# Optimization experiments

Measured on AMD Instinct MI355X. Metric: run time of the kernel, lower is better.

Reference implementation:

```python
import jax, jax.numpy as jnp
import numpy as np

N = 50000      # nodes
E = 600000     # edges
F_IN = 128
F_OUT = 128
R = 4          # num_relations
BN_EPS = 1e-5  # PyTorch BatchNorm1d default


def setup_inputs() -> dict:
    key = jax.random.key(0)
    ks = jax.random.split(key, 8)
    s = 1.0 / np.sqrt(F_IN)
    return {
        "x": jax.random.normal(ks[0], (N, F_IN), jnp.float32),
        "edge_index": jax.random.randint(ks[1], (2, E), 0, N),
        "edge_type": jax.random.randint(ks[2], (E,), 0, R),
        "W_self": jax.random.uniform(ks[3], (F_IN, F_OUT), jnp.float32, -s, s),
        "b_self": jnp.zeros((F_OUT,), jnp.float32),
        "W1": jax.random.uniform(ks[4], (R, F_IN, F_OUT), jnp.float32, -s, s),
        "b1": jnp.zeros((R, F_OUT), jnp.float32),
        "gamma": jnp.ones((R, F_OUT), jnp.float32),
        "beta": jnp.zeros((R, F_OUT), jnp.float32),
        "W2": jax.random.uniform(ks[5], (R, F_OUT, F_OUT), jnp.float32, -s, s),
        "b2": jnp.zeros((R, F_OUT), jnp.float32),
    }


def reference(x, edge_index, edge_type, W_self, b_self, W1, b1, gamma, beta, W2, b2):
    row, col = edge_index[0], edge_index[1]
    # Per-relation scatter-add aggregation in one segment_sum pass:
    # segment id = relation * N + destination row.
    seg = edge_type * N + row
    agg = jax.ops.segment_sum(x[col], seg, num_segments=R * N)
    agg = agg.reshape(R, N, F_IN)
    # GIN update with eps=0: h_r = x + agg_r
    h = x[None, :, :] + agg                              # (R, N, F_IN)
    # Per-relation MLP: Linear -> BatchNorm(train stats) -> ReLU -> Linear
    h = jnp.einsum('rnf,rfo->rno', h, W1) + b1[:, None, :]
    mean = jnp.mean(h, axis=1, keepdims=True)
    var = jnp.var(h, axis=1, keepdims=True)              # biased, as in BN
    h = (h - mean) * jax.lax.rsqrt(var + BN_EPS)
    h = h * gamma[:, None, :] + beta[:, None, :]
    h = jax.nn.relu(h)
    h = jnp.einsum('rno,rop->rnp', h, W2) + b2[:, None, :]
    # Self-loop linear plus sum over relations
    return x @ W_self + b_self + jnp.sum(h, axis=0)
```

## Files before the change

### kernel.cpp

```cpp
#include <hip/hip_runtime.h>

#define Nn 50000
#define Ee 600000
#define Rr 4
#define BN_EPS 1e-5f
#define RCAP 10
#define OVFCAP 256
#define MCAP 128

typedef __bf16 bfrag  __attribute__((ext_vector_type(8)));
typedef float  f32x4  __attribute__((ext_vector_type(4)));

__device__ __forceinline__ unsigned short f2b(float f) {
    union { float f; unsigned int u; } v; v.f = f;
    return (unsigned short)((v.u + 0x7FFFu + ((v.u >> 16) & 1u)) >> 16);
}
__device__ __forceinline__ float b2f(unsigned short u) {
    union { unsigned int u; float f; } v; v.u = ((unsigned int)u) << 16; return v.f;
}

__global__ __launch_bounds__(256) void prep_k(
    const float* __restrict__ x, const float* __restrict__ W1,
    const float* __restrict__ W2, const float* __restrict__ Wself,
    const int* __restrict__ ei, const int* __restrict__ et,
    unsigned int* __restrict__ xb, unsigned short* __restrict__ WT,
    int* __restrict__ rowcnt, unsigned short* __restrict__ bkt,
    int* __restrict__ ovf)
{
    int b = blockIdx.x;
    if (b < 12500) {
        int i = b * 256 + threadIdx.x;
        float2 v = ((const float2*)x)[i];
        xb[i] = ((unsigned int)f2b(v.y) << 16) | f2b(v.x);
    } else if (b < 13076) {
        int idx = (b - 12500) * 256 + threadIdx.x;
        int mat = idx >> 14, rem = idx & 16383;
        int n = rem >> 7, k = rem & 127;
        const float* src = (mat < 4) ? (W1 + mat * 16384)
                         : (mat < 8) ? (W2 + (mat - 4) * 16384) : Wself;
        WT[idx] = f2b(src[k * 128 + n]);
    } else {
        int e = (b - 13076) * 256 + threadIdx.x;
        if (e < Ee) {
            int dst = ei[e], rel = et[e], src = ei[Ee + e];
            int bin = rel * Nn + dst;
            int pos = atomicAdd(&rowcnt[bin], 1);
            if (pos < RCAP) {
                bkt[(size_t)bin * RCAP + pos] = (unsigned short)src;
            } else {
                int op = atomicAdd(&ovf[0], 1);
                if (op < OVFCAP) { ovf[2 + op * 2] = bin; ovf[3 + op * 2] = src; }
            }
        }
    }
}

#define ACC_QUAD(u0_, u1_, u2_, u3_)                                      \
    do {                                                                  \
        unsigned int uu[16] = {u0_.x,u0_.y,u0_.z,u0_.w, u1_.x,u1_.y,u1_.z,u1_.w, \
                               u2_.x,u2_.y,u2_.z,u2_.w, u3_.x,u3_.y,u3_.z,u3_.w}; \
        _Pragma("unroll")                                                 \
        for (int jj = 0; jj < 16; ++jj) {                                 \
            acc[2*jj]   += b2f((unsigned short)(uu[jj] & 0xFFFF));        \
            acc[2*jj+1] += b2f((unsigned short)(uu[jj] >> 16));           \
        }                                                                 \
    } while (0)

__global__ __launch_bounds__(512) void gemm1f_k(
    const unsigned int* __restrict__ xb, const int* __restrict__ rowcnt,
    const unsigned short* __restrict__ bkt, const int* __restrict__ ovf,
    const unsigned short* __restrict__ WT,
    const float* __restrict__ b1, unsigned short* __restrict__ h,
    float* __restrict__ gsum, float* __restrict__ gsq)
{
    const int r  = blockIdx.y;
    const int n0 = blockIdx.x * 128;
    const int t  = threadIdx.x;

    __shared__ __attribute__((aligned(16))) __bf16 As[128][136];
    __shared__ __attribute__((aligned(16))) __bf16 Ws[128][136];
    __shared__ float s_sum[128], s_sq[128];
    __shared__ int s_cnt[128];
    __shared__ int s_edge[128 * RCAP];
    __shared__ int s_mrow[MCAP], s_msrc[MCAP];
    __shared__ int s_on, s_nm;

    const int rows = (Nn - n0 < 128) ? (Nn - n0) : 128;
    const int base = r * Nn + n0;
    if (t < 128) {
        s_sum[t] = 0.f; s_sq[t] = 0.f;
        int c = (t < rows) ? rowcnt[base + t] : 0;
        s_cnt[t] = (c < RCAP) ? c : RCAP;
    }
    {
        const unsigned short* Wr = WT + r * 16384;
        for (int i = t; i < 2048; i += 512) {
            int n = i >> 4, kc = (i & 15) << 3;
            *(uint4*)&Ws[n][kc] = *(const uint4*)(Wr + n * 128 + kc);
        }
    }
    {
        const unsigned int* bp = (const unsigned int*)(bkt + (size_t)base * RCAP);
        for (int i = t; i < (128 * RCAP) / 2; i += 512) {
            int row = i / (RCAP / 2);
            unsigned int u = (row < rows) ? bp[i] : 0u;
            s_edge[2 * i]     = (int)(u & 0xFFFFu);
            s_edge[2 * i + 1] = (int)(u >> 16);
        }
    }
    if (t == 0) {
        int on = ovf[0];
        s_on = (on < OVFCAP) ? on : OVFCAP;
        s_nm = 0;
    }
    __syncthreads();
    if (t < s_on) {
        int bin = ovf[2 + t * 2];
        if (bin >= base && bin < base + rows) {
            int k = atomicAdd(&s_nm, 1);
            if (k < MCAP) { s_mrow[k] = bin - base; s_msrc[k] = ovf[3 + t * 2]; }
        }
    }
    __syncthreads();
    const int nm = (s_nm < MCAP) ? s_nm : MCAP;

    {
        const int row = t >> 2, q = t & 3, gm = n0 + row;
        float acc[32];
#pragma unroll
        for (int j = 0; j < 32; ++j) acc[j] = 0.f;
        if (gm < Nn) {
            const uint4* xr = (const uint4*)(xb + (size_t)gm * 64 + q * 16);
            uint4 u0 = xr[0], u1 = xr[1], u2 = xr[2], u3 = xr[3];
            ACC_QUAD(u0, u1, u2, u3);
            const int je = s_cnt[row];
            const int rb = row * RCAP;
            if (je > 0) {
#define EIDX(jj) (s_edge[rb + ((jj) < je ? (jj) : (je - 1))])
#define EPTR(jj) ((const uint4*)(xb + (size_t)EIDX(jj) * 64 + q * 16))
                const uint4* pA = EPTR(0);
                const uint4* pB = EPTR(1);
                const uint4* pC = EPTR(2);
                uint4 A0 = pA[0], A1 = pA[1], A2 = pA[2], A3 = pA[3];
                uint4 B0 = pB[0], B1 = pB[1], B2 = pB[2], B3 = pB[3];
                uint4 C0 = pC[0], C1 = pC[1], C2 = pC[2], C3 = pC[3];
                for (int j = 0; j < je; j += 3) {
                    ACC_QUAD(A0, A1, A2, A3);
                    { const uint4* p = EPTR(j + 3); A0 = p[0]; A1 = p[1]; A2 = p[2]; A3 = p[3]; }
                    if (j + 1 < je) ACC_QUAD(B0, B1, B2, B3);
                    { const uint4* p = EPTR(j + 4); B0 = p[0]; B1 = p[1]; B2 = p[2]; B3 = p[3]; }
                    if (j + 2 < je) ACC_QUAD(C0, C1, C2, C3);
                    { const uint4* p = EPTR(j + 5); C0 = p[0]; C1 = p[1]; C2 = p[2]; C3 = p[3]; }
                }
#undef EIDX
#undef EPTR
            }
            for (int i = 0; i < nm; ++i) {
                if (s_mrow[i] == row) {
                    const uint4* p = (const uint4*)(xb + (size_t)s_msrc[i] * 64 + q * 16);
                    uint4 o0 = p[0], o1 = p[1], o2 = p[2], o3 = p[3];
                    ACC_QUAD(o0, o1, o2, o3);
                }
            }
        }
        unsigned int pk[16];
#pragma unroll
        for (int j = 0; j < 16; ++j)
            pk[j] = ((unsigned int)f2b(acc[2*j+1]) << 16) | f2b(acc[2*j]);
        uint4* dst = (uint4*)&As[row][q * 32];
        dst[0] = make_uint4(pk[0],  pk[1],  pk[2],  pk[3]);
        dst[1] = make_uint4(pk[4],  pk[5],  pk[6],  pk[7]);
        dst[2] = make_uint4(pk[8],  pk[9],  pk[10], pk[11]);
        dst[3] = make_uint4(pk[12], pk[13], pk[14], pk[15]);
    }
    __syncthreads();

    const int w = t >> 6, l = t & 63, ln = l & 15, quad = l >> 4;
    f32x4 acc2[8];
#pragma unroll
    for (int c = 0; c < 8; ++c) acc2[c] = (f32x4){0.f,0.f,0.f,0.f};
#pragma unroll
    for (int kk = 0; kk < 4; ++kk) {
        int ks = kk * 32 + quad * 8;
        bfrag a = *(const bfrag*)&As[w * 16 + ln][ks];
#pragma unroll
        for (int c = 0; c < 8; ++c) {
            bfrag b = *(const bfrag*)&Ws[c * 16 + ln][ks];
            acc2[c] = __builtin_amdgcn_mfma_f32_16x16x32_bf16(a, b, acc2[c], 0, 0, 0);
        }
    }
    __syncthreads();

#pragma unroll
    for (int c = 0; c < 8; ++c) {
        int col = c * 16 + ln;
        float bias = b1[r * 128 + col];
        float ps = 0.f, pq = 0.f;
#pragma unroll
        for (int reg = 0; reg < 4; ++reg) {
            int lrow = w * 16 + quad * 4 + reg;
            float v = acc2[c][reg] + bias;
            As[lrow][col] = (__bf16)v;
            if (n0 + lrow < Nn) { ps += v; pq += v * v; }
        }
        ps += __shfl_xor(ps, 16); pq += __shfl_xor(pq, 16);
        ps += __shfl_xor(ps, 32); pq += __shfl_xor(pq, 32);
        if (quad == 0) { atomicAdd(&s_sum[col], ps); atomicAdd(&s_sq[col], pq); }
    }
    __syncthreads();

    unsigned short* hr = h + (size_t)r * Nn * 128;
    for (int i = t; i < 2048; i += 512) {
        int m = i >> 4, kc = (i & 15) << 3;
        int gm = n0 + m;
        if (gm < Nn) *(uint4*)(hr + (size_t)gm * 128 + kc) = *(const uint4*)&As[m][kc];
    }
    if (t < 128) {
        atomicAdd(&gsum[r * 128 + t], s_sum[t]);
        atomicAdd(&gsq[r * 128 + t],  s_sq[t]);
    }
}

__global__ void finalize_k(
    const float* __restrict__ gsum, const float* __restrict__ gsq,
    const float* __restrict__ gamma, const float* __restrict__ beta,
    float* __restrict__ coefA, float* __restrict__ coefC)
{
    int i = threadIdx.x;
    float mean = gsum[i] * (1.0f / Nn);
    float var  = gsq[i] * (1.0f / Nn) - mean * mean;
    float a    = gamma[i] * rsqrtf(fmaxf(var, 0.f) + BN_EPS);
    coefA[i] = a;
    coefC[i] = beta[i] - mean * a;
}

__global__ __launch_bounds__(512) void gemm2f_k(
    const unsigned int* __restrict__ xb,
    const unsigned short* __restrict__ h,
    const unsigned short* __restrict__ WT,
    const float* __restrict__ bself, const float* __restrict__ b2,
    const float* __restrict__ coefA, const float* __restrict__ coefC,
    float* __restrict__ out)
{
    const int n0 = blockIdx.x * 128;
    const int t  = threadIdx.x;
    __shared__ __attribute__((aligned(16))) __bf16 As[128][136];
    __shared__ __attribute__((aligned(16))) __bf16 Ws[128][136];

    const int w = t >> 6, l = t & 63, ln = l & 15, quad = l >> 4;
    f32x4 acc2[8];
#pragma unroll
    for (int c = 0; c < 8; ++c) acc2[c] = (f32x4){0.f,0.f,0.f,0.f};

    for (int rr = 0; rr < 5; ++rr) {
        const unsigned short* Wr = WT + (rr < 4 ? (4 + rr) : 8) * 16384;
        for (int i = t; i < 2048; i += 512) {
            int n = i >> 4, kc = (i & 15) << 3;
            *(uint4*)&Ws[n][kc] = *(const uint4*)(Wr + n * 128 + kc);
        }
        if (rr < 4) {
            const unsigned short* hrp = h + (size_t)rr * Nn * 128;
            const float* cA = coefA + rr * 128;
            const float* cC = coefC + rr * 128;
            for (int i = t; i < 2048; i += 512) {
                int m = i >> 4, kc = (i & 15) << 3;
                int gm = n0 + m;
                uint4 hv = make_uint4(0,0,0,0);
                if (gm < Nn) hv = *(const uint4*)(hrp + (size_t)gm * 128 + kc);
                unsigned int hu[4] = {hv.x, hv.y, hv.z, hv.w};
                unsigned int pk[4];
#pragma unroll
                for (int j = 0; j < 4; ++j) {
                    float v0 = fmaxf(cA[kc + 2*j]     * b2f((unsigned short)(hu[j] & 0xFFFF)) + cC[kc + 2*j],     0.f);
                    float v1 = fmaxf(cA[kc + 2*j + 1] * b2f((unsigned short)(hu[j] >> 16))    + cC[kc + 2*j + 1], 0.f);
                    pk[j] = ((unsigned int)f2b(v1) << 16) | f2b(v0);
                }
                *(uint4*)&As[m][kc] = make_uint4(pk[0], pk[1], pk[2], pk[3]);
            }
        } else {
            for (int i = t; i < 2048; i += 512) {
                int m = i >> 4, kc = (i & 15) << 3;
                int gm = n0 + m;
                uint4 v = make_uint4(0, 0, 0, 0);
                if (gm < Nn) v = *(const uint4*)(xb + (size_t)gm * 64 + (kc >> 1));
                *(uint4*)&As[m][kc] = v;
            }
        }
        __syncthreads();
#pragma unroll
        for (int kk = 0; kk < 4; ++kk) {
            int ks = kk * 32 + quad * 8;
            bfrag a = *(const bfrag*)&As[w * 16 + ln][ks];
#pragma unroll
            for (int c = 0; c < 8; ++c) {
                bfrag b = *(const bfrag*)&Ws[c * 16 + ln][ks];
                acc2[c] = __builtin_amdgcn_mfma_f32_16x16x32_bf16(a, b, acc2[c], 0, 0, 0);
            }
        }
        __syncthreads();
    }

    float bias[8];
#pragma unroll
    for (int c = 0; c < 8; ++c) {
        int col = c * 16 + ln;
        bias[c] = bself[col] + b2[col] + b2[128 + col] + b2[256 + col] + b2[384 + col];
    }
    float* fws = (float*)Ws;
    for (int p = 0; p < 2; ++p) {
        if ((w >> 2) == p) {
#pragma unroll
            for (int c = 0; c < 8; ++c) {
                int lrow = (w & 3) * 16 + quad * 4;
                int col  = c * 16 + ln;
#pragma unroll
                for (int reg = 0; reg < 4; ++reg)
                    fws[(lrow + reg) * 132 + col] = acc2[c][reg] + bias[c];
            }
        }
        __syncthreads();
        for (int i = t; i < 2048; i += 512) {
            int m = i >> 5, kc = (i & 31) << 2;
            int gm = n0 + p * 64 + m;
            if (gm < Nn)
                *(float4*)(out + (size_t)gm * 128 + kc) = *(const float4*)&fws[m * 132 + kc];
        }
        __syncthreads();
    }
}

extern "C" void kernel_launch(void* const* d_in, const int* in_sizes, int n_in,
                              void* d_out, int out_size, void* d_ws, size_t ws_size,
                              hipStream_t stream) {
    const float* x     = (const float*)d_in[0];
    const int*   ei    = (const int*)d_in[1];
    const int*   et    = (const int*)d_in[2];
    const float* Wself = (const float*)d_in[3];
    const float* bself = (const float*)d_in[4];
    const float* W1    = (const float*)d_in[5];
    const float* b1    = (const float*)d_in[6];
    const float* gamma = (const float*)d_in[7];
    const float* beta  = (const float*)d_in[8];
    const float* W2    = (const float*)d_in[9];
    const float* b2    = (const float*)d_in[10];
    float* out = (float*)d_out;

    char* ws = (char*)d_ws;
    float* gsum  = (float*)(ws + 0);
    float* gsq   = (float*)(ws + 2048);
    float* coefA = (float*)(ws + 4096);
    float* coefC = (float*)(ws + 6144);
    int*   ovf   = (int*)(ws + 8192);
    int*   rowcnt= (int*)(ws + 16384);
    unsigned short* bkt = (unsigned short*)(ws + 816384);
    unsigned short* h  = (unsigned short*)(ws + 4818688);
    unsigned int*   xb = (unsigned int*)(ws + 56018688);
    unsigned short* WT = (unsigned short*)(ws + 68818688);

    (void)hipMemsetAsync(ws, 0, 816384, stream);

    const int EB = (Ee + 255) / 256;
    prep_k <<<12500 + 576 + EB, 256, 0, stream>>>(x, W1, W2, Wself, ei, et,
                                                  xb, WT, rowcnt, bkt, ovf);

    dim3 g1((Nn + 127) / 128, Rr);
    gemm1f_k<<<g1, 512, 0, stream>>>(xb, rowcnt, bkt, ovf, WT, b1, h, gsum, gsq);
    finalize_k<<<1, 512, 0, stream>>>(gsum, gsq, gamma, beta, coefA, coefC);
    gemm2f_k<<<(Nn + 127) / 128, 512, 0, stream>>>(
        xb, h, WT, bself, b2, coefA, coefC, out);
}
```

Before: 241.4 us.

## Fold BN finalize into second GEMM and halve its row tile

Measured after the change: 244.7 us. Within noise of the previous version (+1.4%).

```diff
diff --git a/kernel.cpp b/kernel.cpp
--- a/kernel.cpp
+++ b/kernel.cpp
@@ -221,36 +221,29 @@
     }
 }
 
-__global__ void finalize_k(
-    const float* __restrict__ gsum, const float* __restrict__ gsq,
-    const float* __restrict__ gamma, const float* __restrict__ beta,
-    float* __restrict__ coefA, float* __restrict__ coefC)
-{
-    int i = threadIdx.x;
-    float mean = gsum[i] * (1.0f / Nn);
-    float var  = gsq[i] * (1.0f / Nn) - mean * mean;
-    float a    = gamma[i] * rsqrtf(fmaxf(var, 0.f) + BN_EPS);
-    coefA[i] = a;
-    coefC[i] = beta[i] - mean * a;
-}
-
 __global__ __launch_bounds__(512) void gemm2f_k(
     const unsigned int* __restrict__ xb,
     const unsigned short* __restrict__ h,
     const unsigned short* __restrict__ WT,
     const float* __restrict__ bself, const float* __restrict__ b2,
-    const float* __restrict__ coefA, const float* __restrict__ coefC,
+    const float* __restrict__ gsum, const float* __restrict__ gsq,
+    const float* __restrict__ gamma, const float* __restrict__ beta,
     float* __restrict__ out)
 {
-    const int n0 = blockIdx.x * 128;
+    const int n0 = blockIdx.x * 64;
     const int t  = threadIdx.x;
-    __shared__ __attribute__((aligned(16))) __bf16 As[128][136];
+    __shared__ __attribute__((aligned(16))) __bf16 As[64][136];
     __shared__ __attribute__((aligned(16))) __bf16 Ws[128][136];
 
     const int w = t >> 6, l = t & 63, ln = l & 15, quad = l >> 4;
-    f32x4 acc2[8];
-#pragma unroll
-    for (int c = 0; c < 8; ++c) acc2[c] = (f32x4){0.f,0.f,0.f,0.f};
+    const int rg = w & 3, ch = w >> 2;
+    f32x4 acc2[4];
+#pragma unroll
+    for (int c = 0; c < 4; ++c) acc2[c] = (f32x4){0.f,0.f,0.f,0.f};
+
+    const int m0  = t >> 4;
+    const int m1  = m0 + 32;
+    const int kc0 = (t & 15) << 3;
 
     for (int rr = 0; rr < 5; ++rr) {
         const unsigned short* Wr = WT + (rr < 4 ? (4 + rr) : 8) * 16384;
@@ -259,73 +252,78 @@
             *(uint4*)&Ws[n][kc] = *(const uint4*)(Wr + n * 128 + kc);
         }
         if (rr < 4) {
+            float cAv[8], cCv[8];
+#pragma unroll
+            for (int j = 0; j < 8; ++j) {
+                int col = rr * 128 + kc0 + j;
+                float mean = gsum[col] * (1.0f / Nn);
+                float var  = gsq[col] * (1.0f / Nn) - mean * mean;
+                float a    = gamma[col] * rsqrtf(fmaxf(var, 0.f) + BN_EPS);
+                cAv[j] = a;
+                cCv[j] = beta[col] - mean * a;
+            }
             const unsigned short* hrp = h + (size_t)rr * Nn * 128;
-            const float* cA = coefA + rr * 128;
-            const float* cC = coefC + rr * 128;
-            for (int i = t; i < 2048; i += 512) {
-                int m = i >> 4, kc = (i & 15) << 3;
+#pragma unroll
+            for (int cc = 0; cc < 2; ++cc) {
+                int m = cc ? m1 : m0;
                 int gm = n0 + m;
                 uint4 hv = make_uint4(0,0,0,0);
-                if (gm < Nn) hv = *(const uint4*)(hrp + (size_t)gm * 128 + kc);
+                if (gm < Nn) hv = *(const uint4*)(hrp + (size_t)gm * 128 + kc0);
                 unsigned int hu[4] = {hv.x, hv.y, hv.z, hv.w};
                 unsigned int pk[4];
 #pragma unroll
                 for (int j = 0; j < 4; ++j) {
-                    float v0 = fmaxf(cA[kc + 2*j]     * b2f((unsigned short)(hu[j] & 0xFFFF)) + cC[kc + 2*j],     0.f);
-                    float v1 = fmaxf(cA[kc + 2*j + 1] * b2f((unsigned short)(hu[j] >> 16))    + cC[kc + 2*j + 1], 0.f);
+                    float v0 = fmaxf(cAv[2*j]     * b2f((unsigned short)(hu[j] & 0xFFFF)) + cCv[2*j],     0.f);
+                    float v1 = fmaxf(cAv[2*j + 1] * b2f((unsigned short)(hu[j] >> 16))    + cCv[2*j + 1], 0.f);
                     pk[j] = ((unsigned int)f2b(v1) << 16) | f2b(v0);
                 }
-                *(uint4*)&As[m][kc] = make_uint4(pk[0], pk[1], pk[2], pk[3]);
+                *(uint4*)&As[m][kc0] = make_uint4(pk[0], pk[1], pk[2], pk[3]);
             }
         } else {
-            for (int i = t; i < 2048; i += 512) {
-                int m = i >> 4, kc = (i & 15) << 3;
+#pragma unroll
+            for (int cc = 0; cc < 2; ++cc) {
+                int m = cc ? m1 : m0;
                 int gm = n0 + m;
                 uint4 v = make_uint4(0, 0, 0, 0);
-                if (gm < Nn) v = *(const uint4*)(xb + (size_t)gm * 64 + (kc >> 1));
-                *(uint4*)&As[m][kc] = v;
+                if (gm < Nn) v = *(const uint4*)(xb + (size_t)gm * 64 + (kc0 >> 1));
+                *(uint4*)&As[m][kc0] = v;
             }
         }
         __syncthreads();
 #pragma unroll
         for (int kk = 0; kk < 4; ++kk) {
             int ks = kk * 32 + quad * 8;
-            bfrag a = *(const bfrag*)&As[w * 16 + ln][ks];
-#pragma unroll
-            for (int c = 0; c < 8; ++c) {
-                bfrag b = *(const bfrag*)&Ws[c * 16 + ln][ks];
+            bfrag a = *(const bfrag*)&As[rg * 16 + ln][ks];
+#pragma unroll
+            for (int c = 0; c < 4; ++c) {
+                bfrag b = *(const bfrag*)&Ws[ch * 64 + c * 16 + ln][ks];
                 acc2[c] = __builtin_amdgcn_mfma_f32_16x16x32_bf16(a, b, acc2[c], 0, 0, 0);
             }
         }
         __syncthreads();
     }
 
-    float bias[8];
-#pragma unroll
-    for (int c = 0; c < 8; ++c) {
-        int col = c * 16 + ln;
+    float bias[4];
+#pragma unroll
+    for (int c = 0; c < 4; ++c) {
+        int col = ch * 64 + c * 16 + ln;
         bias[c] = bself[col] + b2[col] + b2[128 + col] + b2[256 + col] + b2[384 + col];
     }
     float* fws = (float*)Ws;
-    for (int p = 0; p < 2; ++p) {
-        if ((w >> 2) == p) {
-#pragma unroll
-            for (int c = 0; c < 8; ++c) {
-                int lrow = (w & 3) * 16 + quad * 4;
-                int col  = c * 16 + ln;
-#pragma unroll
-                for (int reg = 0; reg < 4; ++reg)
-                    fws[(lrow + reg) * 132 + col] = acc2[c][reg] + bias[c];
-            }
-        }
-        __syncthreads();
-        for (int i = t; i < 2048; i += 512) {
-            int m = i >> 5, kc = (i & 31) << 2;
-            int gm = n0 + p * 64 + m;
-            if (gm < Nn)
-                *(float4*)(out + (size_t)gm * 128 + kc) = *(const float4*)&fws[m * 132 + kc];
-        }
-        __syncthreads();
+#pragma unroll
+    for (int c = 0; c < 4; ++c) {
+        int lrow = rg * 16 + quad * 4;
+        int col  = ch * 64 + c * 16 + ln;
+#pragma unroll
+        for (int reg = 0; reg < 4; ++reg)
+            fws[(lrow + reg) * 132 + col] = acc2[c][reg] + bias[c];
+    }
+    __syncthreads();
+    for (int i = t; i < 2048; i += 512) {
+        int m = i >> 5, kc = (i & 31) << 2;
+        int gm = n0 + m;
+        if (gm < Nn)
+            *(float4*)(out + (size_t)gm * 128 + kc) = *(const float4*)&fws[m * 132 + kc];
     }
 }
 
@@ -348,8 +346,6 @@
     char* ws = (char*)d_ws;
     float* gsum  = (float*)(ws + 0);
     float* gsq   = (float*)(ws + 2048);
-    float* coefA = (float*)(ws + 4096);
-    float* coefC = (float*)(ws + 6144);
     int*   ovf   = (int*)(ws + 8192);
     int*   rowcnt= (int*)(ws + 16384);
     unsigned short* bkt = (unsigned short*)(ws + 816384);
@@ -365,7 +361,6 @@
 
     dim3 g1((Nn + 127) / 128, Rr);
     gemm1f_k<<<g1, 512, 0, stream>>>(xb, rowcnt, bkt, ovf, WT, b1, h, gsum, gsq);
-    finalize_k<<<1, 512, 0, stream>>>(gsum, gsq, gamma, beta, coefA, coefC);
-    gemm2f_k<<<(Nn + 127) / 128, 512, 0, stream>>>(
-        xb, h, WT, bself, b2, coefA, coefC, out);
-}
+    gemm2f_k<<<(Nn + 63) / 64, 512, 0, stream>>>(
+        xb, h, WT, bself, b2, gsum, gsq, gamma, beta, out);
+}
```
